# Kernel tuning notes

Hardware: AMD Instinct MI355X
Metric: run time of the kernel (lower is better)

Reference implementation:

```python
import jax, jax.numpy as jnp
import numpy as np

EPS = 1e-5
RADIUS = 1.0

def bn(x, gamma, beta, axis=1):
    # inference-mode BatchNorm1d: running_mean=0, running_var=1
    shape = [1] * x.ndim
    shape[axis] = -1
    return x * (gamma / jnp.sqrt(1.0 + EPS)).reshape(shape) + beta.reshape(shape)

def pconv(x, w):
    # pointwise Conv1d (kernel_size=1): x [B,Cin,N], w [Cout,Cin]
    return jnp.einsum('oi,bin->bon', w, x)

def sq_dist(a, b):
    # a [B,N,3], b [B,S,3] -> squared pairwise distances [B,N,S]
    return (jnp.sum(a * a, -1)[:, :, None] + jnp.sum(b * b, -1)[:, None, :]
            - 2.0 * jnp.einsum('bnc,bsc->bns', a, b))

def index_points(points, idx):
    # points [B,S,...], idx [B,...] -> gathered [B, idx.shape[1:], ...]
    return jax.vmap(lambda p, i: p[i])(points, idx)

def fps(xyz, npoint):
    # farthest point sampling (deterministic start at index 0)
    B, N, _ = xyz.shape
    binds = jnp.arange(B)
    def step(carry, _):
        dist, far = carry
        c = xyz[binds, far]                                    # [B,3]
        d = jnp.sum((xyz - c[:, None, :]) ** 2, -1)            # [B,N]
        dist = jnp.minimum(dist, d)
        nxt = jnp.argmax(dist, -1).astype(jnp.int32)
        return (dist, nxt), far
    init = (jnp.full((B, N), 1e10, xyz.dtype), jnp.zeros((B,), jnp.int32))
    _, idx = jax.lax.scan(step, init, None, length=npoint)
    return jnp.transpose(idx)                                   # [B,npoint]

def query_ball(radius, nsample, xyz, new_xyz):
    # indices of first nsample points within radius of each center
    B, N, _ = xyz.shape
    S = new_xyz.shape[1]
    d2 = sq_dist(new_xyz, xyz)                                  # [B,S,N]
    gidx = jnp.broadcast_to(jnp.arange(N, dtype=jnp.int32), (B, S, N))
    gidx = jnp.where(d2 > radius * radius, N, gidx)
    gidx = jnp.sort(gidx, axis=-1)[:, :, :nsample]
    first = gidx[:, :, :1]
    gidx = jnp.where(gidx == N, first, gidx)
    return jnp.clip(gidx, 0, N - 1)

def sample_and_group(npoint, nsample, radius, xyz, points):
    fps_idx = fps(xyz, npoint)
    new_xyz = index_points(xyz, fps_idx)                        # [B,S,3]
    new_pts = index_points(points, fps_idx)                     # [B,S,D]
    idx = query_ball(radius, nsample, xyz, new_xyz)             # [B,S,K]
    grouped = index_points(points, idx)                         # [B,S,K,D]
    centered = grouped - new_pts[:, :, None, :]
    rep = jnp.broadcast_to(new_pts[:, :, None, :], centered.shape)
    return new_xyz, jnp.concatenate([centered, rep], axis=-1)   # [B,S,K,2D]

def local_op(x, w1, g1, b1, w2, g2, b2):
    # x [B,n,K,d]; shared pointwise MLP over channels then max over K
    h = jnp.einsum('oi,bnki->bnok', w1, x)
    h = jax.nn.relu(bn(h, g1, b1, axis=2))
    h = jnp.einsum('oi,bnik->bnok', w2, h)
    h = jax.nn.relu(bn(h, g2, b2, axis=2))
    return jnp.transpose(jnp.max(h, -1), (0, 2, 1))             # [B,out,n]

def feature_prop(xyz1, xyz2, points1, points2, w1, g1, b1, w2, g2, b2):
    # 3-NN inverse-distance interpolation of points2 onto xyz1, concat points1
    p1 = jnp.transpose(xyz1, (0, 2, 1))                         # [B,N,3]
    p2 = jnp.transpose(xyz2, (0, 2, 1))                         # [B,S,3]
    f2 = jnp.transpose(points2, (0, 2, 1))                      # [B,S,D2]
    negd, idx = jax.lax.top_k(-sq_dist(p1, p2), 3)              # [B,N,3]
    recip = 1.0 / (-negd + 1e-8)
    w = recip / jnp.sum(recip, -1, keepdims=True)
    interp = jnp.sum(index_points(f2, idx) * w[..., None], 2)   # [B,N,D2]
    new = jnp.concatenate([points1, jnp.transpose(interp, (0, 2, 1))], axis=1)
    new = jax.nn.relu(bn(pconv(new, w1), g1, b1))
    new = jax.nn.relu(bn(pconv(new, w2), g2, b2))
    return new


def setup_inputs() -> dict:
    key = jax.random.key(0)
    ks = iter(jax.random.split(key, 80))
    def W(*s):  return jax.random.normal(next(ks), s, jnp.float32) * 0.05
    def G(n):   return 1.0 + 0.1 * jax.random.normal(next(ks), (n,), jnp.float32)
    def Bt(n):  return 0.1 * jax.random.normal(next(ks), (n,), jnp.float32)
    inp = {"x": jax.random.uniform(next(ks), (4, 8192, 3), jnp.float32)}
    inp.update(w_emb1=W(64, 3), g_emb1=G(64), be_emb1=Bt(64),
               w_emb2=W(64, 64), g_emb2=G(64), be_emb2=Bt(64),
               l0_w1=W(128, 128), l0_g1=G(128), l0_b1=Bt(128),
               l0_w2=W(128, 128), l0_g2=G(128), l0_b2=Bt(128),
               l1_w1=W(256, 256), l1_g1=G(256), l1_b1=Bt(256),
               l1_w2=W(256, 256), l1_g2=G(256), l1_b2=Bt(256),
               f0_w1=W(256, 384), f0_g1=G(256), f0_b1=Bt(256),
               f0_w2=W(512, 256), f0_g2=G(512), f0_b2=Bt(512),
               f1_w1=W(512, 576), f1_g1=G(512), f1_b1=Bt(512),
               f1_w2=W(1024, 512), f1_g2=G(1024), f1_b2=Bt(1024),
               c1_w=W(512, 1024), c1_bias=Bt(512), c1_g=G(512), c1_beta=Bt(512),
               c2_w=W(128, 512), c2_bias=Bt(128), c2_g=G(128), c2_beta=Bt(128),
               out_w=W(8, 128), out_bias=Bt(8))
    return inp


def reference(x, w_emb1, g_emb1, be_emb1, w_emb2, g_emb2, be_emb2,
              l0_w1, l0_g1, l0_b1, l0_w2, l0_g2, l0_b2,
              l1_w1, l1_g1, l1_b1, l1_w2, l1_g2, l1_b2,
              f0_w1, f0_g1, f0_b1, f0_w2, f0_g2, f0_b2,
              f1_w1, f1_g1, f1_b1, f1_w2, f1_g2, f1_b2,
              c1_w, c1_bias, c1_g, c1_beta, c2_w, c2_bias, c2_g, c2_beta,
              out_w, out_bias):
    xyz = x                                                     # [B,N,3]
    h = jnp.transpose(x, (0, 2, 1))                             # [B,3,N]
    h = jax.nn.relu(bn(pconv(h, w_emb1), g_emb1, be_emb1))
    h = jax.nn.relu(bn(pconv(h, w_emb2), g_emb2, be_emb2))
    feats0 = h                                                  # [B,64,N]
    xyz1, g1f = sample_and_group(2048, 32, RADIUS, xyz, jnp.transpose(h, (0, 2, 1)))
    feats1 = local_op(g1f, l0_w1, l0_g1, l0_b1, l0_w2, l0_g2, l0_b2)   # [B,128,2048]
    xyz2, g2f = sample_and_group(1024, 32, RADIUS, xyz1, jnp.transpose(feats1, (0, 2, 1)))
    feats2 = local_op(g2f, l1_w1, l1_g1, l1_b1, l1_w2, l1_g2, l1_b2)   # [B,256,1024]
    h = feature_prop(jnp.transpose(xyz1, (0, 2, 1)), jnp.transpose(xyz2, (0, 2, 1)),
                     feats1, feats2, f0_w1, f0_g1, f0_b1, f0_w2, f0_g2, f0_b2)   # [B,512,2048]
    h = feature_prop(jnp.transpose(xyz, (0, 2, 1)), jnp.transpose(xyz1, (0, 2, 1)),
                     feats0, h, f1_w1, f1_g1, f1_b1, f1_w2, f1_g2, f1_b2)        # [B,1024,N]
    h = jax.nn.relu(bn(pconv(h, c1_w) + c1_bias[None, :, None], c1_g, c1_beta))
    h = jax.nn.relu(bn(pconv(h, c2_w) + c2_bias[None, :, None], c2_g, c2_beta))
    logits = pconv(h, out_w) + out_bias[None, :, None]
    return jnp.transpose(logits, (0, 2, 1))                     # [B,N,labels]
```

## Files before the change

### kernel.cpp

```cpp
#include <hip/hip_runtime.h>
#include <math.h>


static constexpr size_t O_FEATS0 = 0;
static constexpr size_t O_FEATS1 = 8388608;
static constexpr size_t O_FEATS2 = 12582912;
static constexpr size_t O_FP0OUT = 16777216;
static constexpr size_t O_XYZ1   = 33554432;
static constexpr size_t O_XYZ2   = 33652736;
static constexpr size_t O_FPS1   = 33701888;
static constexpr size_t O_FPS2   = 33734656;
static constexpr size_t O_BALL1  = 33751040;
static constexpr size_t O_BALL2  = 34799616;
static constexpr size_t O_NN0I   = 35323904;
static constexpr size_t O_NN0W   = 35422208;
static constexpr size_t O_NN1I   = 35520512;
static constexpr size_t O_NN1W   = 35913728;
static constexpr size_t O_REG0   = 36306944;
static constexpr size_t O_REG1   = 103415808;
static constexpr size_t WS_NEED  = 170524672;

typedef float v2f __attribute__((ext_vector_type(2)));

__global__ __launch_bounds__(256) void emb_kernel(
    const float* __restrict__ xyz, const float* __restrict__ w1,
    const float* __restrict__ g1, const float* __restrict__ b1,
    const float* __restrict__ w2, const float* __restrict__ g2,
    const float* __restrict__ b2, float* __restrict__ out) {
  const int t = threadIdx.x;
  const int o = t & 63, pl = t >> 6;
  const int pt = blockIdx.x * 4 + pl;
  const float x0 = xyz[(size_t)pt * 3 + 0];
  const float x1 = xyz[(size_t)pt * 3 + 1];
  const float x2 = xyz[(size_t)pt * 3 + 2];
  const float SQ = sqrtf(1.0f + 1e-5f);
  float v = w1[o * 3 + 0] * x0 + w1[o * 3 + 1] * x1 + w1[o * 3 + 2] * x2;
  v = fmaxf(v * (g1[o] / SQ) + b1[o], 0.0f);
  __shared__ float h[4][64];
  h[pl][o] = v;
  __syncthreads();
  float acc = 0.0f;
  #pragma unroll 8
  for (int i = 0; i < 64; ++i) acc += w2[o * 64 + i] * h[pl][i];
  float y = fmaxf(acc * (g2[o] / SQ) + b2[o], 0.0f);
  out[(size_t)pt * 64 + o] = y;
}

__device__ __forceinline__ unsigned long long u64max(unsigned long long a,
                                                     unsigned long long b) {
  return a > b ? a : b;
}
template <int CTRL>
__device__ __forceinline__ unsigned long long dpp_step(unsigned long long k) {
  const int lo = (int)(unsigned)k;
  const int hi = (int)(unsigned)(k >> 32);
  const int nlo = __builtin_amdgcn_update_dpp(lo, lo, CTRL, 0xf, 0xf, false);
  const int nhi = __builtin_amdgcn_update_dpp(hi, hi, CTRL, 0xf, 0xf, false);
  return ((unsigned long long)(unsigned)nhi << 32) | (unsigned)nlo;
}

template <int N, int NP>
__global__ __launch_bounds__(256, 1) void fps_kernel(
    const float* __restrict__ xyz, int* __restrict__ out,
    float* __restrict__ oxyz) {
  #pragma clang fp contract(off)
  constexpr int PPT = N / 256;
  constexpr int PAIRS = PPT / 2;
  const int b = blockIdx.x, t = threadIdx.x;
  const float* xb = xyz + (size_t)b * N * 3;
  __shared__ float sx[N], sy[N], sz[N];
  __shared__ int sfar[NP];
  __shared__ unsigned long long skey[2][4];
  for (int i = t; i < N; i += 256) {
    sx[i] = xb[i * 3 + 0];
    sy[i] = xb[i * 3 + 1];
    sz[i] = xb[i * 3 + 2];
  }
  __syncthreads();
  v2f px[PAIRS], py[PAIRS], pz[PAIRS], ds[PAIRS];
  #pragma unroll
  for (int k = 0; k < PAIRS; ++k) {
    const int g = t * PPT + 2 * k;
    px[k].x = sx[g]; px[k].y = sx[g + 1];
    py[k].x = sy[g]; py[k].y = sy[g + 1];
    pz[k].x = sz[g]; pz[k].y = sz[g + 1];
    ds[k].x = 1e10f; ds[k].y = 1e10f;
  }
  const int wid = t >> 6, lane = t & 63;
  int far = 0;
  float ccx = sx[0], ccy = sy[0], ccz = sz[0];
  for (int it = 0; it < NP; ++it) {
    if (t == 0) sfar[it] = far;
    v2f cx2, cy2, cz2;
    cx2.x = ccx; cx2.y = ccx;
    cy2.x = ccy; cy2.y = ccy;
    cz2.x = ccz; cz2.y = ccz;
    #pragma unroll
    for (int k = 0; k < PAIRS; ++k) {
      const v2f dx = px[k] - cx2;
      const v2f dy = py[k] - cy2;
      const v2f dz = pz[k] - cz2;
      const v2f d = dx * dx + dy * dy + dz * dz;
      v2f nd;
      nd.x = fminf(ds[k].x, d.x);
      nd.y = fminf(ds[k].y, d.y);
      ds[k] = nd;
    }
    v2f tv[PAIRS / 2];
    #pragma unroll
    for (int k = 0; k < PAIRS / 2; ++k) {
      tv[k].x = fmaxf(ds[k].x, ds[k + PAIRS / 2].x);
      tv[k].y = fmaxf(ds[k].y, ds[k + PAIRS / 2].y);
    }
    #pragma unroll
    for (int w = PAIRS / 4; w >= 1; w >>= 1) {
      #pragma unroll
      for (int k = 0; k < w; ++k) {
        tv[k].x = fmaxf(tv[k].x, tv[k + w].x);
        tv[k].y = fmaxf(tv[k].y, tv[k + w].y);
      }
    }
    const float bv = fmaxf(tv[0].x, tv[0].y);
    unsigned mask = 0u;
    #pragma unroll
    for (int k = 0; k < PAIRS; ++k) {
      mask |= (ds[k].x == bv) ? (1u << (2 * k)) : 0u;
      mask |= (ds[k].y == bv) ? (1u << (2 * k + 1)) : 0u;
    }
    const int bjl = __builtin_ctz(mask);
    unsigned long long bk =
        ((unsigned long long)__float_as_uint(bv) << 32) |
        (unsigned long long)(unsigned)(~(unsigned)(t * PPT + bjl));
    bk = u64max(bk, dpp_step<0x111>(bk));
    bk = u64max(bk, dpp_step<0x112>(bk));
    bk = u64max(bk, dpp_step<0x114>(bk));
    bk = u64max(bk, dpp_step<0x118>(bk));
    bk = u64max(bk, dpp_step<0x142>(bk));
    bk = u64max(bk, dpp_step<0x143>(bk));
    const int p = it & 1;
    if (lane == 63) skey[p][wid] = bk;
    __syncthreads();
    unsigned long long wk = skey[p][0];
    #pragma unroll
    for (int q = 1; q < 4; ++q) {
      const unsigned long long k2 = skey[p][q];
      wk = (k2 > wk) ? k2 : wk;
    }
    far = (int)(~(unsigned)wk);
    ccx = sx[far]; ccy = sy[far]; ccz = sz[far];
  }
  __syncthreads();
  for (int i = t; i < NP; i += 256) {
    const int n = sfar[i];
    out[(size_t)b * NP + i] = n;
    oxyz[((size_t)b * NP + i) * 3 + 0] = sx[n];
    oxyz[((size_t)b * NP + i) * 3 + 1] = sy[n];
    oxyz[((size_t)b * NP + i) * 3 + 2] = sz[n];
  }
}

__global__ __launch_bounds__(256) void ball_kernel(
    const float* __restrict__ xyz, const float* __restrict__ ctr,
    int* __restrict__ out, int sbits, int N) {
  const int t = threadIdx.x;
  const int lane = t & 63, wid = t >> 6;
  const int wg = blockIdx.x * 4 + wid;
  const int b = wg >> sbits;
  __shared__ int lists[4][32];
  const float cx = ctr[(size_t)wg * 3 + 0];
  const float cy = ctr[(size_t)wg * 3 + 1];
  const float cz = ctr[(size_t)wg * 3 + 2];
  const float an = __fadd_rn(__fadd_rn(__fmul_rn(cx, cx), __fmul_rn(cy, cy)),
                             __fmul_rn(cz, cz));
  int fill = 0;
  for (int ch = 0; ch < (N >> 6) && fill < 32; ++ch) {
    const int n = ch * 64 + lane;
    const float bx = xyz[((size_t)b * N + n) * 3 + 0];
    const float by = xyz[((size_t)b * N + n) * 3 + 1];
    const float bz = xyz[((size_t)b * N + n) * 3 + 2];
    const float bb = __fadd_rn(__fadd_rn(__fmul_rn(bx, bx), __fmul_rn(by, by)),
                               __fmul_rn(bz, bz));
    const float dot = __fadd_rn(__fadd_rn(__fmul_rn(cx, bx), __fmul_rn(cy, by)),
                                __fmul_rn(cz, bz));
    const float d2 = __fsub_rn(__fadd_rn(an, bb), __fmul_rn(2.0f, dot));
    const bool q = (d2 <= 1.0f);
    const unsigned long long mask = __ballot(q);
    if (q) {
      const int pos = fill + __popcll(mask & ((1ull << lane) - 1ull));
      if (pos < 32) lists[wid][pos] = n;
    }
    fill += (int)__popcll(mask);
  }
  __syncthreads();
  if (lane < 32) {
    int v = lists[wid][0];
    if (lane < fill) v = lists[wid][lane];
    out[(size_t)wg * 32 + lane] = v;
  }
}

__global__ __launch_bounds__(256) void groupmat_kernel(
    float* __restrict__ Xo, const float* __restrict__ f,
    const int* __restrict__ ball, const int* __restrict__ fps, int g0, int Cf,
    int c4bits, int sbits, int Npts) {
  const int id = blockIdx.x * 256 + threadIdx.x;
  const int c4mask = (1 << c4bits) - 1;
  const int row = id >> c4bits;
  const int col = (id & c4mask) * 4;
  const int gl = g0 + (row >> 5);
  const int k = row & 31;
  const int b = gl >> sbits;
  const int src = ball[(size_t)gl * 32 + k];
  const int ctr = fps[gl];
  const int C = Cf * 2;
  const float* fb = f + (size_t)b * Npts * Cf;
  float4 v;
  if (col < Cf) {
    const float4 a = *(const float4*)(fb + (size_t)src * Cf + col);
    const float4 c = *(const float4*)(fb + (size_t)ctr * Cf + col);
    v = make_float4(a.x - c.x, a.y - c.y, a.z - c.z, a.w - c.w);
  } else {
    v = *(const float4*)(fb + (size_t)ctr * Cf + (col - Cf));
  }
  *(float4*)(Xo + (size_t)row * C + col) = v;
}

#define CMAP(c) ((((c) >> 3) * 12) + ((c) & 7))
__global__ __launch_bounds__(256) void conv_kernel(
    const float* __restrict__ X, const float* __restrict__ W,
    float* __restrict__ Y, int C, int O, const float* __restrict__ gamma,
    const float* __restrict__ beta, const float* __restrict__ bias, int relu) {
  __shared__ float Xs[16][188];
  __shared__ float Ws[16][188];
  const int t = threadIdx.x;
  const size_t m0 = (size_t)blockIdx.x * 128;
  const int o0 = blockIdx.y * 128;
  const int r0 = t >> 2;
  const int cq0 = (t & 3) * 4;
  const int mq = t & 15, nq = t >> 4;
  const int ca = CMAP(r0), cb = CMAP(r0 + 64);
  v2f acc[8][4];
  #pragma unroll
  for (int i = 0; i < 8; ++i)
    #pragma unroll
    for (int j = 0; j < 4; ++j) acc[i][j] = (v2f){0.0f, 0.0f};

  for (int kk = 0; kk < C; kk += 16) {
    const float4 xa = *(const float4*)(X + (m0 + r0) * C + kk + cq0);
    const float4 xb = *(const float4*)(X + (m0 + r0 + 64) * C + kk + cq0);
    const float4 wa = *(const float4*)(W + (size_t)(o0 + r0) * C + kk + cq0);
    const float4 wb = *(const float4*)(W + (size_t)(o0 + r0 + 64) * C + kk + cq0);
    __syncthreads();
    Xs[cq0 + 0][ca] = xa.x; Xs[cq0 + 1][ca] = xa.y;
    Xs[cq0 + 2][ca] = xa.z; Xs[cq0 + 3][ca] = xa.w;
    Xs[cq0 + 0][cb] = xb.x; Xs[cq0 + 1][cb] = xb.y;
    Xs[cq0 + 2][cb] = xb.z; Xs[cq0 + 3][cb] = xb.w;
    Ws[cq0 + 0][ca] = wa.x; Ws[cq0 + 1][ca] = wa.y;
    Ws[cq0 + 2][ca] = wa.z; Ws[cq0 + 3][ca] = wa.w;
    Ws[cq0 + 0][cb] = wb.x; Ws[cq0 + 1][cb] = wb.y;
    Ws[cq0 + 2][cb] = wb.z; Ws[cq0 + 3][cb] = wb.w;
    __syncthreads();
    #pragma unroll
    for (int k = 0; k < 16; ++k) {
      const float4 a0 = *(const float4*)&Xs[k][mq * 12];
      const float4 a1 = *(const float4*)&Xs[k][mq * 12 + 4];
      const float4 b0 = *(const float4*)&Ws[k][nq * 12];
      const float4 b1 = *(const float4*)&Ws[k][nq * 12 + 4];
      const float am[8] = {a0.x, a0.y, a0.z, a0.w, a1.x, a1.y, a1.z, a1.w};
      v2f bv[4];
      bv[0] = (v2f){b0.x, b0.y};
      bv[1] = (v2f){b0.z, b0.w};
      bv[2] = (v2f){b1.x, b1.y};
      bv[3] = (v2f){b1.z, b1.w};
      #pragma unroll
      for (int i = 0; i < 8; ++i) {
        const v2f as = (v2f){am[i], am[i]};
        #pragma unroll
        for (int j = 0; j < 4; ++j) acc[i][j] += as * bv[j];
      }
    }
  }

  const float SQ = sqrtf(1.0f + 1e-5f);
  float s[8], sh[8];
  #pragma unroll
  for (int j = 0; j < 8; ++j) {
    const int o = o0 + nq * 8 + j;
    const float sc = gamma ? (gamma[o] / SQ) : 1.0f;
    float bb = beta ? beta[o] : 0.0f;
    if (bias) bb = bb + bias[o] * sc;
    s[j] = sc; sh[j] = bb;
  }
  #pragma unroll
  for (int i = 0; i < 8; ++i) {
    float y[8];
    #pragma unroll
    for (int j = 0; j < 4; ++j) {
      float va = acc[i][j].x * s[2 * j] + sh[2 * j];
      float vb = acc[i][j].y * s[2 * j + 1] + sh[2 * j + 1];
      y[2 * j] = relu ? fmaxf(va, 0.0f) : va;
      y[2 * j + 1] = relu ? fmaxf(vb, 0.0f) : vb;
    }
    const size_t off = (m0 + mq * 8 + i) * O + o0 + nq * 8;
    *(float4*)(Y + off) = make_float4(y[0], y[1], y[2], y[3]);
    *(float4*)(Y + off + 4) = make_float4(y[4], y[5], y[6], y[7]);
  }
}

__global__ __launch_bounds__(256) void segmax_kernel(
    const float* __restrict__ Y, float* __restrict__ F, int O, int obits) {
  const int id = blockIdx.x * 256 + threadIdx.x;
  const int g = id >> obits;
  const int o = id & (O - 1);
  float m = -3.4e38f;
  #pragma unroll 8
  for (int k = 0; k < 32; ++k)
    m = fmaxf(m, Y[((size_t)g * 32 + k) * O + o]);
  F[(size_t)g * O + o] = m;
}

__global__ __launch_bounds__(256) void nn3_kernel(
    const float* __restrict__ txyz, const float* __restrict__ sxyz,
    int* __restrict__ oi, float* __restrict__ ow, int s1bits, int S2) {
  __shared__ float ss[6144];
  const int t = threadIdx.x;
  const int row = blockIdx.x * 256 + t;
  const int b = row >> s1bits;
  for (int i = t; i < S2 * 3; i += 256) ss[i] = sxyz[(size_t)b * S2 * 3 + i];
  __syncthreads();
  const float ax = txyz[(size_t)row * 3 + 0];
  const float ay = txyz[(size_t)row * 3 + 1];
  const float az = txyz[(size_t)row * 3 + 2];
  const float an = __fadd_rn(__fadd_rn(__fmul_rn(ax, ax), __fmul_rn(ay, ay)),
                             __fmul_rn(az, az));
  float d0 = 3.4e38f, d1 = 3.4e38f, d2v = 3.4e38f;
  int i0 = 0, i1 = 0, i2 = 0;
  for (int j = 0; j < S2; ++j) {
    const float bx = ss[j * 3 + 0], by = ss[j * 3 + 1], bz = ss[j * 3 + 2];
    const float bb = __fadd_rn(__fadd_rn(__fmul_rn(bx, bx), __fmul_rn(by, by)),
                               __fmul_rn(bz, bz));
    const float dot = __fadd_rn(__fadd_rn(__fmul_rn(ax, bx), __fmul_rn(ay, by)),
                                __fmul_rn(az, bz));
    const float dd = __fsub_rn(__fadd_rn(an, bb), __fmul_rn(2.0f, dot));
    if (dd < d0) {
      d2v = d1; i2 = i1; d1 = d0; i1 = i0; d0 = dd; i0 = j;
    } else if (dd < d1) {
      d2v = d1; i2 = i1; d1 = dd; i1 = j;
    } else if (dd < d2v) {
      d2v = dd; i2 = j;
    }
  }
  const float r0 = 1.0f / (d0 + 1e-8f);
  const float r1 = 1.0f / (d1 + 1e-8f);
  const float r2 = 1.0f / (d2v + 1e-8f);
  const float sum = __fadd_rn(__fadd_rn(r0, r1), r2);
  oi[(size_t)row * 3 + 0] = i0;
  oi[(size_t)row * 3 + 1] = i1;
  oi[(size_t)row * 3 + 2] = i2;
  ow[(size_t)row * 3 + 0] = r0 / sum;
  ow[(size_t)row * 3 + 1] = r1 / sum;
  ow[(size_t)row * 3 + 2] = r2 / sum;
}

__global__ __launch_bounds__(256) void interp_kernel(
    float* __restrict__ dst, int CT, int c0, const float* __restrict__ src,
    const int* __restrict__ idx, const float* __restrict__ w, int csbits,
    int s1bits, int S2) {
  const int id = blockIdx.x * 256 + threadIdx.x;
  const int row = id >> csbits;
  const int c4 = (id & ((1 << csbits) - 1)) * 4;
  const int Cs = 4 << csbits;
  const int b = row >> s1bits;
  const int j0 = idx[(size_t)row * 3 + 0];
  const int j1 = idx[(size_t)row * 3 + 1];
  const int j2 = idx[(size_t)row * 3 + 2];
  const float w0 = w[(size_t)row * 3 + 0];
  const float w1 = w[(size_t)row * 3 + 1];
  const float w2 = w[(size_t)row * 3 + 2];
  const float4 f0 = *(const float4*)(src + ((size_t)b * S2 + j0) * Cs + c4);
  const float4 f1 = *(const float4*)(src + ((size_t)b * S2 + j1) * Cs + c4);
  const float4 f2 = *(const float4*)(src + ((size_t)b * S2 + j2) * Cs + c4);
  float4 v;
  v.x = f0.x * w0 + f1.x * w1 + f2.x * w2;
  v.y = f0.y * w0 + f1.y * w1 + f2.y * w2;
  v.z = f0.z * w0 + f1.z * w1 + f2.z * w2;
  v.w = f0.w * w0 + f1.w * w1 + f2.w * w2;
  *(float4*)(dst + (size_t)row * CT + c0 + c4) = v;
}

__global__ __launch_bounds__(256) void copycols_kernel(
    float* __restrict__ dst, int CT, int c0, const float* __restrict__ src,
    int csbits) {
  const int id = blockIdx.x * 256 + threadIdx.x;
  const int row = id >> csbits;
  const int c4 = (id & ((1 << csbits) - 1)) * 4;
  const int Cs = 4 << csbits;
  const float4 v = *(const float4*)(src + (size_t)row * Cs + c4);
  *(float4*)(dst + (size_t)row * CT + c0 + c4) = v;
}

__global__ __launch_bounds__(256) void outfinal_kernel(
    const float* __restrict__ X, const float* __restrict__ Wt,
    const float* __restrict__ bias, float* __restrict__ out) {
  __shared__ float Xs[32][132];
  const int t = threadIdx.x;
  const int p0 = blockIdx.x * 32;
  #pragma unroll
  for (int q = 0; q < 4; ++q) {
    const int id = t + q * 256;
    const int r = id >> 5, c4 = (id & 31) * 4;
    const float4 v = *(const float4*)(X + (size_t)(p0 + r) * 128 + c4);
    Xs[r][c4 + 0] = v.x; Xs[r][c4 + 1] = v.y;
    Xs[r][c4 + 2] = v.z; Xs[r][c4 + 3] = v.w;
  }
  __syncthreads();
  const int p = t >> 3, o = t & 7;
  float acc = 0.0f;
  #pragma unroll 8
  for (int i = 0; i < 128; ++i) acc += Wt[o * 128 + i] * Xs[p][i];
  out[(size_t)(p0 + p) * 8 + o] = acc + bias[o];
}

extern "C" void kernel_launch(void* const* d_in, const int* in_sizes, int n_in,
                              void* d_out, int out_size, void* d_ws,
                              size_t ws_size, hipStream_t stream) {
  const float* x       = (const float*)d_in[0];
  const float* w_emb1  = (const float*)d_in[1];
  const float* g_emb1  = (const float*)d_in[2];
  const float* be_emb1 = (const float*)d_in[3];
  const float* w_emb2  = (const float*)d_in[4];
  const float* g_emb2  = (const float*)d_in[5];
  const float* be_emb2 = (const float*)d_in[6];
  const float* l0_w1 = (const float*)d_in[7];
  const float* l0_g1 = (const float*)d_in[8];
  const float* l0_b1 = (const float*)d_in[9];
  const float* l0_w2 = (const float*)d_in[10];
  const float* l0_g2 = (const float*)d_in[11];
  const float* l0_b2 = (const float*)d_in[12];
  const float* l1_w1 = (const float*)d_in[13];
  const float* l1_g1 = (const float*)d_in[14];
  const float* l1_b1 = (const float*)d_in[15];
  const float* l1_w2 = (const float*)d_in[16];
  const float* l1_g2 = (const float*)d_in[17];
  const float* l1_b2 = (const float*)d_in[18];
  const float* f0_w1 = (const float*)d_in[19];
  const float* f0_g1 = (const float*)d_in[20];
  const float* f0_b1 = (const float*)d_in[21];
  const float* f0_w2 = (const float*)d_in[22];
  const float* f0_g2 = (const float*)d_in[23];
  const float* f0_b2 = (const float*)d_in[24];
  const float* f1_w1 = (const float*)d_in[25];
  const float* f1_g1 = (const float*)d_in[26];
  const float* f1_b1 = (const float*)d_in[27];
  const float* f1_w2 = (const float*)d_in[28];
  const float* f1_g2 = (const float*)d_in[29];
  const float* f1_b2 = (const float*)d_in[30];
  const float* c1_w    = (const float*)d_in[31];
  const float* c1_bias = (const float*)d_in[32];
  const float* c1_g    = (const float*)d_in[33];
  const float* c1_beta = (const float*)d_in[34];
  const float* c2_w    = (const float*)d_in[35];
  const float* c2_bias = (const float*)d_in[36];
  const float* c2_g    = (const float*)d_in[37];
  const float* c2_beta = (const float*)d_in[38];
  const float* out_w    = (const float*)d_in[39];
  const float* out_bias = (const float*)d_in[40];

  if (ws_size < WS_NEED) return;

  char* ws = (char*)d_ws;
  float* feats0 = (float*)(ws + O_FEATS0);
  float* feats1 = (float*)(ws + O_FEATS1);
  float* feats2 = (float*)(ws + O_FEATS2);
  float* fp0out = (float*)(ws + O_FP0OUT);
  float* xyz1   = (float*)(ws + O_XYZ1);
  float* xyz2   = (float*)(ws + O_XYZ2);
  int*   fps1   = (int*)(ws + O_FPS1);
  int*   fps2   = (int*)(ws + O_FPS2);
  int*   ball1  = (int*)(ws + O_BALL1);
  int*   ball2  = (int*)(ws + O_BALL2);
  int*   nn0i   = (int*)(ws + O_NN0I);
  float* nn0w   = (float*)(ws + O_NN0W);
  int*   nn1i   = (int*)(ws + O_NN1I);
  float* nn1w   = (float*)(ws + O_NN1W);
  float* REG0   = (float*)(ws + O_REG0);
  float* REG1   = (float*)(ws + O_REG1);
  float* outp   = (float*)d_out;
  hipStream_t s = stream;

  emb_kernel<<<8192, 256, 0, s>>>(x, w_emb1, g_emb1, be_emb1, w_emb2, g_emb2,
                                  be_emb2, feats0);

  fps_kernel<8192, 2048><<<4, 256, 0, s>>>(x, fps1, xyz1);
  ball_kernel<<<2048, 256, 0, s>>>(x, xyz1, ball1, 11, 8192);
  for (int c = 0; c < 2; ++c) {
    groupmat_kernel<<<16384, 256, 0, s>>>(REG0, feats0, ball1, fps1, c * 4096,
                                          64, 5, 11, 8192);
    conv_kernel<<<dim3(1024, 1), 256, 0, s>>>(REG0, l0_w1, REG1, 128, 128,
                                              l0_g1, l0_b1, nullptr, 1);
    conv_kernel<<<dim3(1024, 1), 256, 0, s>>>(REG1, l0_w2, REG0, 128, 128,
                                              l0_g2, l0_b2, nullptr, 1);
    segmax_kernel<<<2048, 256, 0, s>>>(REG0, feats1 + (size_t)c * 4096 * 128,
                                       128, 7);
  }

  fps_kernel<2048, 1024><<<4, 256, 0, s>>>(xyz1, fps2, xyz2);
  ball_kernel<<<1024, 256, 0, s>>>(xyz1, xyz2, ball2, 10, 2048);
  for (int c = 0; c < 2; ++c) {
    groupmat_kernel<<<16384, 256, 0, s>>>(REG0, feats1, ball2, fps2, c * 2048,
                                          128, 6, 10, 2048);
    conv_kernel<<<dim3(512, 2), 256, 0, s>>>(REG0, l1_w1, REG1, 256, 256,
                                             l1_g1, l1_b1, nullptr, 1);
    conv_kernel<<<dim3(512, 2), 256, 0, s>>>(REG1, l1_w2, REG0, 256, 256,
                                             l1_g2, l1_b2, nullptr, 1);
    segmax_kernel<<<2048, 256, 0, s>>>(REG0, feats2 + (size_t)c * 2048 * 256,
                                       256, 8);
  }

  nn3_kernel<<<32, 256, 0, s>>>(xyz1, xyz2, nn0i, nn0w, 11, 1024);
  copycols_kernel<<<1024, 256, 0, s>>>(REG0, 384, 0, feats1, 5);
  interp_kernel<<<2048, 256, 0, s>>>(REG0, 384, 128, feats2, nn0i, nn0w, 6, 11,
                                     1024);
  conv_kernel<<<dim3(64, 2), 256, 0, s>>>(REG0, f0_w1, REG1, 384, 256, f0_g1,
                                          f0_b1, nullptr, 1);
  conv_kernel<<<dim3(64, 4), 256, 0, s>>>(REG1, f0_w2, fp0out, 256, 512, f0_g2,
                                          f0_b2, nullptr, 1);

  nn3_kernel<<<128, 256, 0, s>>>(x, xyz1, nn1i, nn1w, 13, 2048);
  for (int b = 0; b < 4; b += 2) {
    copycols_kernel<<<1024, 256, 0, s>>>(REG0, 576, 0,
                                         feats0 + (size_t)b * 8192 * 64, 4);
    interp_kernel<<<8192, 256, 0, s>>>(REG0, 576, 64,
                                       fp0out + (size_t)b * 2048 * 512,
                                       nn1i + (size_t)b * 8192 * 3,
                                       nn1w + (size_t)b * 8192 * 3, 7, 13,
                                       2048);
    conv_kernel<<<dim3(128, 4), 256, 0, s>>>(REG0, f1_w1, REG1, 576, 512,
                                             f1_g1, f1_b1, nullptr, 1);
    conv_kernel<<<dim3(128, 8), 256, 0, s>>>(REG1, f1_w2, REG0, 512, 1024,
                                             f1_g2, f1_b2, nullptr, 1);
    conv_kernel<<<dim3(128, 4), 256, 0, s>>>(REG0, c1_w, REG1, 1024, 512,
                                             c1_g, c1_beta, c1_bias, 1);
    conv_kernel<<<dim3(128, 1), 256, 0, s>>>(REG1, c2_w, REG0, 512, 128,
                                             c2_g, c2_beta, c2_bias, 1);
    outfinal_kernel<<<512, 256, 0, s>>>(REG0, out_w, out_bias,
                                        outp + (size_t)b * 8192 * 8);
  }
}
```

Baseline: 4.995 ms.

## Fuse group gather into conv, segmax into second conv, co-launch emb/fps and ball/nn

Folds the grouping gather into the first local conv so the grouped matrix is never written to global memory. Folds the segment max into the epilogue of the second conv so the full per-neighbour output is never written. Runs the embedding MLP as extra blocks of the FPS launch so it fills the idle CUs while four FPS blocks run serially. Ball query and 3-NN are merged into one launch in the same way. This removes several large global round trips and launches, but the conv tile's X load now becomes an indirect gather, and FPS shares a launch with many short blocks.

```diff
diff --git a/kernel.cpp b/kernel.cpp
--- a/kernel.cpp
+++ b/kernel.cpp
@@ -22,30 +22,6 @@
 
 typedef float v2f __attribute__((ext_vector_type(2)));
 
-__global__ __launch_bounds__(256) void emb_kernel(
-    const float* __restrict__ xyz, const float* __restrict__ w1,
-    const float* __restrict__ g1, const float* __restrict__ b1,
-    const float* __restrict__ w2, const float* __restrict__ g2,
-    const float* __restrict__ b2, float* __restrict__ out) {
-  const int t = threadIdx.x;
-  const int o = t & 63, pl = t >> 6;
-  const int pt = blockIdx.x * 4 + pl;
-  const float x0 = xyz[(size_t)pt * 3 + 0];
-  const float x1 = xyz[(size_t)pt * 3 + 1];
-  const float x2 = xyz[(size_t)pt * 3 + 2];
-  const float SQ = sqrtf(1.0f + 1e-5f);
-  float v = w1[o * 3 + 0] * x0 + w1[o * 3 + 1] * x1 + w1[o * 3 + 2] * x2;
-  v = fmaxf(v * (g1[o] / SQ) + b1[o], 0.0f);
-  __shared__ float h[4][64];
-  h[pl][o] = v;
-  __syncthreads();
-  float acc = 0.0f;
-  #pragma unroll 8
-  for (int i = 0; i < 64; ++i) acc += w2[o * 64 + i] * h[pl][i];
-  float y = fmaxf(acc * (g2[o] / SQ) + b2[o], 0.0f);
-  out[(size_t)pt * 64 + o] = y;
-}
-
 __device__ __forceinline__ unsigned long long u64max(unsigned long long a,
                                                      unsigned long long b) {
   return a > b ? a : b;
@@ -59,18 +35,47 @@
   return ((unsigned long long)(unsigned)nhi << 32) | (unsigned)nlo;
 }
 
-template <int N, int NP>
+template <int N, int NP, bool EMB>
 __global__ __launch_bounds__(256, 1) void fps_kernel(
     const float* __restrict__ xyz, int* __restrict__ out,
-    float* __restrict__ oxyz) {
+    float* __restrict__ oxyz, const float* __restrict__ w1,
+    const float* __restrict__ g1, const float* __restrict__ b1,
+    const float* __restrict__ w2, const float* __restrict__ g2,
+    const float* __restrict__ b2, float* __restrict__ femb) {
   #pragma clang fp contract(off)
   constexpr int PPT = N / 256;
   constexpr int PAIRS = PPT / 2;
-  const int b = blockIdx.x, t = threadIdx.x;
-  const float* xb = xyz + (size_t)b * N * 3;
   __shared__ float sx[N], sy[N], sz[N];
   __shared__ int sfar[NP];
   __shared__ unsigned long long skey[2][4];
+
+  if constexpr (EMB) {
+    if (blockIdx.x >= 4) {
+      #pragma clang fp contract(fast)
+      const int bid = blockIdx.x - 4;
+      const int t = threadIdx.x;
+      const int o = t & 63, pl = t >> 6;
+      const int pt = bid * 4 + pl;
+      const float x0 = xyz[(size_t)pt * 3 + 0];
+      const float x1 = xyz[(size_t)pt * 3 + 1];
+      const float x2 = xyz[(size_t)pt * 3 + 2];
+      const float SQ = sqrtf(1.0f + 1e-5f);
+      float v = w1[o * 3 + 0] * x0 + w1[o * 3 + 1] * x1 + w1[o * 3 + 2] * x2;
+      v = fmaxf(v * (g1[o] / SQ) + b1[o], 0.0f);
+      float* h = sx;
+      h[pl * 64 + o] = v;
+      __syncthreads();
+      float acc = 0.0f;
+      #pragma unroll 8
+      for (int i = 0; i < 64; ++i) acc += w2[o * 64 + i] * h[pl * 64 + i];
+      float y = fmaxf(acc * (g2[o] / SQ) + b2[o], 0.0f);
+      femb[(size_t)pt * 64 + o] = y;
+      return;
+    }
+  }
+
+  const int b = blockIdx.x, t = threadIdx.x;
+  const float* xb = xyz + (size_t)b * N * 3;
   for (int i = t; i < N; i += 256) {
     sx[i] = xb[i * 3 + 0];
     sy[i] = xb[i * 3 + 1];
@@ -159,172 +164,51 @@
   }
 }
 
-__global__ __launch_bounds__(256) void ball_kernel(
-    const float* __restrict__ xyz, const float* __restrict__ ctr,
-    int* __restrict__ out, int sbits, int N) {
-  const int t = threadIdx.x;
-  const int lane = t & 63, wid = t >> 6;
-  const int wg = blockIdx.x * 4 + wid;
-  const int b = wg >> sbits;
-  __shared__ int lists[4][32];
-  const float cx = ctr[(size_t)wg * 3 + 0];
-  const float cy = ctr[(size_t)wg * 3 + 1];
-  const float cz = ctr[(size_t)wg * 3 + 2];
-  const float an = __fadd_rn(__fadd_rn(__fmul_rn(cx, cx), __fmul_rn(cy, cy)),
-                             __fmul_rn(cz, cz));
-  int fill = 0;
-  for (int ch = 0; ch < (N >> 6) && fill < 32; ++ch) {
-    const int n = ch * 64 + lane;
-    const float bx = xyz[((size_t)b * N + n) * 3 + 0];
-    const float by = xyz[((size_t)b * N + n) * 3 + 1];
-    const float bz = xyz[((size_t)b * N + n) * 3 + 2];
-    const float bb = __fadd_rn(__fadd_rn(__fmul_rn(bx, bx), __fmul_rn(by, by)),
-                               __fmul_rn(bz, bz));
-    const float dot = __fadd_rn(__fadd_rn(__fmul_rn(cx, bx), __fmul_rn(cy, by)),
-                                __fmul_rn(cz, bz));
-    const float d2 = __fsub_rn(__fadd_rn(an, bb), __fmul_rn(2.0f, dot));
-    const bool q = (d2 <= 1.0f);
-    const unsigned long long mask = __ballot(q);
-    if (q) {
-      const int pos = fill + __popcll(mask & ((1ull << lane) - 1ull));
-      if (pos < 32) lists[wid][pos] = n;
-    }
-    fill += (int)__popcll(mask);
-  }
-  __syncthreads();
-  if (lane < 32) {
-    int v = lists[wid][0];
-    if (lane < fill) v = lists[wid][lane];
-    out[(size_t)wg * 32 + lane] = v;
-  }
-}
-
-__global__ __launch_bounds__(256) void groupmat_kernel(
-    float* __restrict__ Xo, const float* __restrict__ f,
-    const int* __restrict__ ball, const int* __restrict__ fps, int g0, int Cf,
-    int c4bits, int sbits, int Npts) {
-  const int id = blockIdx.x * 256 + threadIdx.x;
-  const int c4mask = (1 << c4bits) - 1;
-  const int row = id >> c4bits;
-  const int col = (id & c4mask) * 4;
-  const int gl = g0 + (row >> 5);
-  const int k = row & 31;
-  const int b = gl >> sbits;
-  const int src = ball[(size_t)gl * 32 + k];
-  const int ctr = fps[gl];
-  const int C = Cf * 2;
-  const float* fb = f + (size_t)b * Npts * Cf;
-  float4 v;
-  if (col < Cf) {
-    const float4 a = *(const float4*)(fb + (size_t)src * Cf + col);
-    const float4 c = *(const float4*)(fb + (size_t)ctr * Cf + col);
-    v = make_float4(a.x - c.x, a.y - c.y, a.z - c.z, a.w - c.w);
-  } else {
-    v = *(const float4*)(fb + (size_t)ctr * Cf + (col - Cf));
-  }
-  *(float4*)(Xo + (size_t)row * C + col) = v;
-}
-
-#define CMAP(c) ((((c) >> 3) * 12) + ((c) & 7))
-__global__ __launch_bounds__(256) void conv_kernel(
-    const float* __restrict__ X, const float* __restrict__ W,
-    float* __restrict__ Y, int C, int O, const float* __restrict__ gamma,
-    const float* __restrict__ beta, const float* __restrict__ bias, int relu) {
-  __shared__ float Xs[16][188];
-  __shared__ float Ws[16][188];
-  const int t = threadIdx.x;
-  const size_t m0 = (size_t)blockIdx.x * 128;
-  const int o0 = blockIdx.y * 128;
-  const int r0 = t >> 2;
-  const int cq0 = (t & 3) * 4;
-  const int mq = t & 15, nq = t >> 4;
-  const int ca = CMAP(r0), cb = CMAP(r0 + 64);
-  v2f acc[8][4];
-  #pragma unroll
-  for (int i = 0; i < 8; ++i)
-    #pragma unroll
-    for (int j = 0; j < 4; ++j) acc[i][j] = (v2f){0.0f, 0.0f};
-
-  for (int kk = 0; kk < C; kk += 16) {
-    const float4 xa = *(const float4*)(X + (m0 + r0) * C + kk + cq0);
-    const float4 xb = *(const float4*)(X + (m0 + r0 + 64) * C + kk + cq0);
-    const float4 wa = *(const float4*)(W + (size_t)(o0 + r0) * C + kk + cq0);
-    const float4 wb = *(const float4*)(W + (size_t)(o0 + r0 + 64) * C + kk + cq0);
-    __syncthreads();
-    Xs[cq0 + 0][ca] = xa.x; Xs[cq0 + 1][ca] = xa.y;
-    Xs[cq0 + 2][ca] = xa.z; Xs[cq0 + 3][ca] = xa.w;
-    Xs[cq0 + 0][cb] = xb.x; Xs[cq0 + 1][cb] = xb.y;
-    Xs[cq0 + 2][cb] = xb.z; Xs[cq0 + 3][cb] = xb.w;
-    Ws[cq0 + 0][ca] = wa.x; Ws[cq0 + 1][ca] = wa.y;
-    Ws[cq0 + 2][ca] = wa.z; Ws[cq0 + 3][ca] = wa.w;
-    Ws[cq0 + 0][cb] = wb.x; Ws[cq0 + 1][cb] = wb.y;
-    Ws[cq0 + 2][cb] = wb.z; Ws[cq0 + 3][cb] = wb.w;
-    __syncthreads();
-    #pragma unroll
-    for (int k = 0; k < 16; ++k) {
-      const float4 a0 = *(const float4*)&Xs[k][mq * 12];
-      const float4 a1 = *(const float4*)&Xs[k][mq * 12 + 4];
-      const float4 b0 = *(const float4*)&Ws[k][nq * 12];
-      const float4 b1 = *(const float4*)&Ws[k][nq * 12 + 4];
-      const float am[8] = {a0.x, a0.y, a0.z, a0.w, a1.x, a1.y, a1.z, a1.w};
-      v2f bv[4];
-      bv[0] = (v2f){b0.x, b0.y};
-      bv[1] = (v2f){b0.z, b0.w};
-      bv[2] = (v2f){b1.x, b1.y};
-      bv[3] = (v2f){b1.z, b1.w};
-      #pragma unroll
-      for (int i = 0; i < 8; ++i) {
-        const v2f as = (v2f){am[i], am[i]};
-        #pragma unroll
-        for (int j = 0; j < 4; ++j) acc[i][j] += as * bv[j];
-      }
-    }
-  }
-
-  const float SQ = sqrtf(1.0f + 1e-5f);
-  float s[8], sh[8];
-  #pragma unroll
-  for (int j = 0; j < 8; ++j) {
-    const int o = o0 + nq * 8 + j;
-    const float sc = gamma ? (gamma[o] / SQ) : 1.0f;
-    float bb = beta ? beta[o] : 0.0f;
-    if (bias) bb = bb + bias[o] * sc;
-    s[j] = sc; sh[j] = bb;
-  }
-  #pragma unroll
-  for (int i = 0; i < 8; ++i) {
-    float y[8];
-    #pragma unroll
-    for (int j = 0; j < 4; ++j) {
-      float va = acc[i][j].x * s[2 * j] + sh[2 * j];
-      float vb = acc[i][j].y * s[2 * j + 1] + sh[2 * j + 1];
-      y[2 * j] = relu ? fmaxf(va, 0.0f) : va;
-      y[2 * j + 1] = relu ? fmaxf(vb, 0.0f) : vb;
-    }
-    const size_t off = (m0 + mq * 8 + i) * O + o0 + nq * 8;
-    *(float4*)(Y + off) = make_float4(y[0], y[1], y[2], y[3]);
-    *(float4*)(Y + off + 4) = make_float4(y[4], y[5], y[6], y[7]);
-  }
-}
-
-__global__ __launch_bounds__(256) void segmax_kernel(
-    const float* __restrict__ Y, float* __restrict__ F, int O, int obits) {
-  const int id = blockIdx.x * 256 + threadIdx.x;
-  const int g = id >> obits;
-  const int o = id & (O - 1);
-  float m = -3.4e38f;
-  #pragma unroll 8
-  for (int k = 0; k < 32; ++k)
-    m = fmaxf(m, Y[((size_t)g * 32 + k) * O + o]);
-  F[(size_t)g * O + o] = m;
-}
-
-__global__ __launch_bounds__(256) void nn3_kernel(
+__global__ __launch_bounds__(256) void ballnn_kernel(
+    const float* __restrict__ cloud, const float* __restrict__ ctr,
+    int* __restrict__ ballOut, int sbits, int N, int nBallBlk,
     const float* __restrict__ txyz, const float* __restrict__ sxyz,
     int* __restrict__ oi, float* __restrict__ ow, int s1bits, int S2) {
+  __shared__ int lists[4][32];
   __shared__ float ss[6144];
   const int t = threadIdx.x;
-  const int row = blockIdx.x * 256 + t;
+  if ((int)blockIdx.x < nBallBlk) {
+    const int lane = t & 63, wid = t >> 6;
+    const int wg = blockIdx.x * 4 + wid;
+    const int b = wg >> sbits;
+    const float cx = ctr[(size_t)wg * 3 + 0];
+    const float cy = ctr[(size_t)wg * 3 + 1];
+    const float cz = ctr[(size_t)wg * 3 + 2];
+    const float an = __fadd_rn(__fadd_rn(__fmul_rn(cx, cx), __fmul_rn(cy, cy)),
+                               __fmul_rn(cz, cz));
+    int fill = 0;
+    for (int ch = 0; ch < (N >> 6) && fill < 32; ++ch) {
+      const int n = ch * 64 + lane;
+      const float bx = cloud[((size_t)b * N + n) * 3 + 0];
+      const float by = cloud[((size_t)b * N + n) * 3 + 1];
+      const float bz = cloud[((size_t)b * N + n) * 3 + 2];
+      const float bb = __fadd_rn(
+          __fadd_rn(__fmul_rn(bx, bx), __fmul_rn(by, by)), __fmul_rn(bz, bz));
+      const float dot = __fadd_rn(
+          __fadd_rn(__fmul_rn(cx, bx), __fmul_rn(cy, by)), __fmul_rn(cz, bz));
+      const float d2 = __fsub_rn(__fadd_rn(an, bb), __fmul_rn(2.0f, dot));
+      const bool q = (d2 <= 1.0f);
+      const unsigned long long mask = __ballot(q);
+      if (q) {
+        const int pos = fill + __popcll(mask & ((1ull << lane) - 1ull));
+        if (pos < 32) lists[wid][pos] = n;
+      }
+      fill += (int)__popcll(mask);
+    }
+    __syncthreads();
+    if (lane < 32) {
+      int v = lists[wid][0];
+      if (lane < fill) v = lists[wid][lane];
+      ballOut[(size_t)wg * 32 + lane] = v;
+    }
+    return;
+  }
+  const int row = (blockIdx.x - nBallBlk) * 256 + t;
   const int b = row >> s1bits;
   for (int i = t; i < S2 * 3; i += 256) ss[i] = sxyz[(size_t)b * S2 * 3 + i];
   __syncthreads();
@@ -360,6 +244,291 @@
   ow[(size_t)row * 3 + 0] = r0 / sum;
   ow[(size_t)row * 3 + 1] = r1 / sum;
   ow[(size_t)row * 3 + 2] = r2 / sum;
+}
+
+#define CMAP(c) ((((c) >> 3) * 12) + ((c) & 7))
+
+__global__ __launch_bounds__(256) void conv_gather_kernel(
+    const float* __restrict__ f, const int* __restrict__ ball,
+    const int* __restrict__ fps, int g0, int Cf, int sbits, int Npts,
+    const float* __restrict__ W, float* __restrict__ Y, int O,
+    const float* __restrict__ gamma, const float* __restrict__ beta) {
+  const int C = Cf * 2;
+  __shared__ float Xs[16][188];
+  __shared__ float Ws[16][188];
+  const int t = threadIdx.x;
+  const size_t m0 = (size_t)blockIdx.x * 128;
+  const int o0 = blockIdx.y * 128;
+  const int r0 = t >> 2;
+  const int cq0 = (t & 3) * 4;
+  const int mq = t & 15, nq = t >> 4;
+  const int ca = CMAP(r0), cb = CMAP(r0 + 64);
+  const int mA = (int)m0 + r0, mB = (int)m0 + r0 + 64;
+  const int glA = g0 + (mA >> 5), glB = g0 + (mB >> 5);
+  const int srcA = ball[(size_t)glA * 32 + (mA & 31)];
+  const int srcB = ball[(size_t)glB * 32 + (mB & 31)];
+  const int ctrA = fps[glA], ctrB = fps[glB];
+  const float* fbA = f + (size_t)(glA >> sbits) * Npts * Cf;
+  const float* fbB = f + (size_t)(glB >> sbits) * Npts * Cf;
+  v2f acc[8][4];
+  #pragma unroll
+  for (int i = 0; i < 8; ++i)
+    #pragma unroll
+    for (int j = 0; j < 4; ++j) acc[i][j] = (v2f){0.0f, 0.0f};
+
+  for (int kk = 0; kk < C; kk += 16) {
+    const int col = kk + cq0;
+    const bool lo = col < Cf;
+    const int col2 = lo ? col : col - Cf;
+    float4 xa, xb;
+    {
+      const float4 c4 = *(const float4*)(fbA + (size_t)ctrA * Cf + col2);
+      if (lo) {
+        const float4 s4 = *(const float4*)(fbA + (size_t)srcA * Cf + col);
+        xa = make_float4(s4.x - c4.x, s4.y - c4.y, s4.z - c4.z, s4.w - c4.w);
+      } else {
+        xa = c4;
+      }
+    }
+    {
+      const float4 c4 = *(const float4*)(fbB + (size_t)ctrB * Cf + col2);
+      if (lo) {
+        const float4 s4 = *(const float4*)(fbB + (size_t)srcB * Cf + col);
+        xb = make_float4(s4.x - c4.x, s4.y - c4.y, s4.z - c4.z, s4.w - c4.w);
+      } else {
+        xb = c4;
+      }
+    }
+    const float4 wa = *(const float4*)(W + (size_t)(o0 + r0) * C + kk + cq0);
+    const float4 wb =
+        *(const float4*)(W + (size_t)(o0 + r0 + 64) * C + kk + cq0);
+    __syncthreads();
+    Xs[cq0 + 0][ca] = xa.x; Xs[cq0 + 1][ca] = xa.y;
+    Xs[cq0 + 2][ca] = xa.z; Xs[cq0 + 3][ca] = xa.w;
+    Xs[cq0 + 0][cb] = xb.x; Xs[cq0 + 1][cb] = xb.y;
+    Xs[cq0 + 2][cb] = xb.z; Xs[cq0 + 3][cb] = xb.w;
+    Ws[cq0 + 0][ca] = wa.x; Ws[cq0 + 1][ca] = wa.y;
+    Ws[cq0 + 2][ca] = wa.z; Ws[cq0 + 3][ca] = wa.w;
+    Ws[cq0 + 0][cb] = wb.x; Ws[cq0 + 1][cb] = wb.y;
+    Ws[cq0 + 2][cb] = wb.z; Ws[cq0 + 3][cb] = wb.w;
+    __syncthreads();
+    #pragma unroll
+    for (int k = 0; k < 16; ++k) {
+      const float4 a0 = *(const float4*)&Xs[k][mq * 12];
+      const float4 a1 = *(const float4*)&Xs[k][mq * 12 + 4];
+      const float4 b0 = *(const float4*)&Ws[k][nq * 12];
+      const float4 b1 = *(const float4*)&Ws[k][nq * 12 + 4];
+      const float am[8] = {a0.x, a0.y, a0.z, a0.w, a1.x, a1.y, a1.z, a1.w};
+      v2f bv[4];
+      bv[0] = (v2f){b0.x, b0.y};
+      bv[1] = (v2f){b0.z, b0.w};
+      bv[2] = (v2f){b1.x, b1.y};
+      bv[3] = (v2f){b1.z, b1.w};
+      #pragma unroll
+      for (int i = 0; i < 8; ++i) {
+        const v2f as = (v2f){am[i], am[i]};
+        #pragma unroll
+        for (int j = 0; j < 4; ++j) acc[i][j] += as * bv[j];
+      }
+    }
+  }
+
+  const float SQ = sqrtf(1.0f + 1e-5f);
+  float s[8], sh[8];
+  #pragma unroll
+  for (int j = 0; j < 8; ++j) {
+    const int o = o0 + nq * 8 + j;
+    s[j] = gamma[o] / SQ;
+    sh[j] = beta[o];
+  }
+  #pragma unroll
+  for (int i = 0; i < 8; ++i) {
+    float y[8];
+    #pragma unroll
+    for (int j = 0; j < 4; ++j) {
+      y[2 * j] = fmaxf(acc[i][j].x * s[2 * j] + sh[2 * j], 0.0f);
+      y[2 * j + 1] = fmaxf(acc[i][j].y * s[2 * j + 1] + sh[2 * j + 1], 0.0f);
+    }
+    const size_t off = (m0 + mq * 8 + i) * O + o0 + nq * 8;
+    *(float4*)(Y + off) = make_float4(y[0], y[1], y[2], y[3]);
+    *(float4*)(Y + off + 4) = make_float4(y[4], y[5], y[6], y[7]);
+  }
+}
+
+__global__ __launch_bounds__(256) void conv2sm_kernel(
+    const float* __restrict__ X, const float* __restrict__ W,
+    float* __restrict__ F, int C, int O, const float* __restrict__ gamma,
+    const float* __restrict__ beta) {
+  __shared__ float Xs[16][188];
+  __shared__ float Ws[16][188];
+  const int t = threadIdx.x;
+  const size_t m0 = (size_t)blockIdx.x * 128;
+  const int o0 = blockIdx.y * 128;
+  const int r0 = t >> 2;
+  const int cq0 = (t & 3) * 4;
+  const int mq = t & 15, nq = t >> 4;
+  const int ca = CMAP(r0), cb = CMAP(r0 + 64);
+  v2f acc[8][4];
+  #pragma unroll
+  for (int i = 0; i < 8; ++i)
+    #pragma unroll
+    for (int j = 0; j < 4; ++j) acc[i][j] = (v2f){0.0f, 0.0f};
+
+  for (int kk = 0; kk < C; kk += 16) {
+    const float4 xa = *(const float4*)(X + (m0 + r0) * C + kk + cq0);
+    const float4 xb = *(const float4*)(X + (m0 + r0 + 64) * C + kk + cq0);
+    const float4 wa = *(const float4*)(W + (size_t)(o0 + r0) * C + kk + cq0);
+    const float4 wb =
+        *(const float4*)(W + (size_t)(o0 + r0 + 64) * C + kk + cq0);
+    __syncthreads();
+    Xs[cq0 + 0][ca] = xa.x; Xs[cq0 + 1][ca] = xa.y;
+    Xs[cq0 + 2][ca] = xa.z; Xs[cq0 + 3][ca] = xa.w;
+    Xs[cq0 + 0][cb] = xb.x; Xs[cq0 + 1][cb] = xb.y;
+    Xs[cq0 + 2][cb] = xb.z; Xs[cq0 + 3][cb] = xb.w;
+    Ws[cq0 + 0][ca] = wa.x; Ws[cq0 + 1][ca] = wa.y;
+    Ws[cq0 + 2][ca] = wa.z; Ws[cq0 + 3][ca] = wa.w;
+    Ws[cq0 + 0][cb] = wb.x; Ws[cq0 + 1][cb] = wb.y;
+    Ws[cq0 + 2][cb] = wb.z; Ws[cq0 + 3][cb] = wb.w;
+    __syncthreads();
+    #pragma unroll
+    for (int k = 0; k < 16; ++k) {
+      const float4 a0 = *(const float4*)&Xs[k][mq * 12];
+      const float4 a1 = *(const float4*)&Xs[k][mq * 12 + 4];
+      const float4 b0 = *(const float4*)&Ws[k][nq * 12];
+      const float4 b1 = *(const float4*)&Ws[k][nq * 12 + 4];
+      const float am[8] = {a0.x, a0.y, a0.z, a0.w, a1.x, a1.y, a1.z, a1.w};
+      v2f bv[4];
+      bv[0] = (v2f){b0.x, b0.y};
+      bv[1] = (v2f){b0.z, b0.w};
+      bv[2] = (v2f){b1.x, b1.y};
+      bv[3] = (v2f){b1.z, b1.w};
+      #pragma unroll
+      for (int i = 0; i < 8; ++i) {
+        const v2f as = (v2f){am[i], am[i]};
+        #pragma unroll
+        for (int j = 0; j < 4; ++j) acc[i][j] += as * bv[j];
+      }
+    }
+  }
+
+  const float SQ = sqrtf(1.0f + 1e-5f);
+  float s[8], sh[8];
+  #pragma unroll
+  for (int j = 0; j < 8; ++j) {
+    const int o = o0 + nq * 8 + j;
+    s[j] = gamma[o] / SQ;
+    sh[j] = beta[o];
+  }
+  float colmax[8];
+  #pragma unroll
+  for (int j = 0; j < 8; ++j) colmax[j] = -3.4e38f;
+  #pragma unroll
+  for (int i = 0; i < 8; ++i) {
+    #pragma unroll
+    for (int j = 0; j < 4; ++j) {
+      const float va = fmaxf(acc[i][j].x * s[2 * j] + sh[2 * j], 0.0f);
+      const float vb = fmaxf(acc[i][j].y * s[2 * j + 1] + sh[2 * j + 1], 0.0f);
+      colmax[2 * j] = fmaxf(colmax[2 * j], va);
+      colmax[2 * j + 1] = fmaxf(colmax[2 * j + 1], vb);
+    }
+  }
+  __syncthreads();
+  float* smax = &Xs[0][0];
+  #pragma unroll
+  for (int j = 0; j < 8; ++j) smax[mq * 132 + nq * 8 + j] = colmax[j];
+  __syncthreads();
+  #pragma unroll
+  for (int q = 0; q < 2; ++q) {
+    const int idx = t + q * 256;
+    const int g = idx >> 7;
+    const int col = idx & 127;
+    const float m =
+        fmaxf(fmaxf(smax[(4 * g + 0) * 132 + col], smax[(4 * g + 1) * 132 + col]),
+              fmaxf(smax[(4 * g + 2) * 132 + col], smax[(4 * g + 3) * 132 + col]));
+    F[(size_t)(blockIdx.x * 4 + g) * O + o0 + col] = m;
+  }
+}
+
+__global__ __launch_bounds__(256) void conv_kernel(
+    const float* __restrict__ X, const float* __restrict__ W,
+    float* __restrict__ Y, int C, int O, const float* __restrict__ gamma,
+    const float* __restrict__ beta, const float* __restrict__ bias, int relu) {
+  __shared__ float Xs[16][188];
+  __shared__ float Ws[16][188];
+  const int t = threadIdx.x;
+  const size_t m0 = (size_t)blockIdx.x * 128;
+  const int o0 = blockIdx.y * 128;
+  const int r0 = t >> 2;
+  const int cq0 = (t & 3) * 4;
+  const int mq = t & 15, nq = t >> 4;
+  const int ca = CMAP(r0), cb = CMAP(r0 + 64);
+  v2f acc[8][4];
+  #pragma unroll
+  for (int i = 0; i < 8; ++i)
+    #pragma unroll
+    for (int j = 0; j < 4; ++j) acc[i][j] = (v2f){0.0f, 0.0f};
+
+  for (int kk = 0; kk < C; kk += 16) {
+    const float4 xa = *(const float4*)(X + (m0 + r0) * C + kk + cq0);
+    const float4 xb = *(const float4*)(X + (m0 + r0 + 64) * C + kk + cq0);
+    const float4 wa = *(const float4*)(W + (size_t)(o0 + r0) * C + kk + cq0);
+    const float4 wb =
+        *(const float4*)(W + (size_t)(o0 + r0 + 64) * C + kk + cq0);
+    __syncthreads();
+    Xs[cq0 + 0][ca] = xa.x; Xs[cq0 + 1][ca] = xa.y;
+    Xs[cq0 + 2][ca] = xa.z; Xs[cq0 + 3][ca] = xa.w;
+    Xs[cq0 + 0][cb] = xb.x; Xs[cq0 + 1][cb] = xb.y;
+    Xs[cq0 + 2][cb] = xb.z; Xs[cq0 + 3][cb] = xb.w;
+    Ws[cq0 + 0][ca] = wa.x; Ws[cq0 + 1][ca] = wa.y;
+    Ws[cq0 + 2][ca] = wa.z; Ws[cq0 + 3][ca] = wa.w;
+    Ws[cq0 + 0][cb] = wb.x; Ws[cq0 + 1][cb] = wb.y;
+    Ws[cq0 + 2][cb] = wb.z; Ws[cq0 + 3][cb] = wb.w;
+    __syncthreads();
+    #pragma unroll
+    for (int k = 0; k < 16; ++k) {
+      const float4 a0 = *(const float4*)&Xs[k][mq * 12];
+      const float4 a1 = *(const float4*)&Xs[k][mq * 12 + 4];
+      const float4 b0 = *(const float4*)&Ws[k][nq * 12];
+      const float4 b1 = *(const float4*)&Ws[k][nq * 12 + 4];
+      const float am[8] = {a0.x, a0.y, a0.z, a0.w, a1.x, a1.y, a1.z, a1.w};
+      v2f bv[4];
+      bv[0] = (v2f){b0.x, b0.y};
+      bv[1] = (v2f){b0.z, b0.w};
+      bv[2] = (v2f){b1.x, b1.y};
+      bv[3] = (v2f){b1.z, b1.w};
+      #pragma unroll
+      for (int i = 0; i < 8; ++i) {
+        const v2f as = (v2f){am[i], am[i]};
+        #pragma unroll
+        for (int j = 0; j < 4; ++j) acc[i][j] += as * bv[j];
+      }
+    }
+  }
+
+  const float SQ = sqrtf(1.0f + 1e-5f);
+  float s[8], sh[8];
+  #pragma unroll
+  for (int j = 0; j < 8; ++j) {
+    const int o = o0 + nq * 8 + j;
+    const float sc = gamma ? (gamma[o] / SQ) : 1.0f;
+    float bb = beta ? beta[o] : 0.0f;
+    if (bias) bb = bb + bias[o] * sc;
+    s[j] = sc; sh[j] = bb;
+  }
+  #pragma unroll
+  for (int i = 0; i < 8; ++i) {
+    float y[8];
+    #pragma unroll
+    for (int j = 0; j < 4; ++j) {
+      float va = acc[i][j].x * s[2 * j] + sh[2 * j];
+      float vb = acc[i][j].y * s[2 * j + 1] + sh[2 * j + 1];
+      y[2 * j] = relu ? fmaxf(va, 0.0f) : va;
+      y[2 * j + 1] = relu ? fmaxf(vb, 0.0f) : vb;
+    }
+    const size_t off = (m0 + mq * 8 + i) * O + o0 + nq * 8;
+    *(float4*)(Y + off) = make_float4(y[0], y[1], y[2], y[3]);
+    *(float4*)(Y + off + 4) = make_float4(y[4], y[5], y[6], y[7]);
+  }
 }
 
 __global__ __launch_bounds__(256) void interp_kernel(
@@ -488,36 +657,35 @@
   float* outp   = (float*)d_out;
   hipStream_t s = stream;
 
-  emb_kernel<<<8192, 256, 0, s>>>(x, w_emb1, g_emb1, be_emb1, w_emb2, g_emb2,
-                                  be_emb2, feats0);
-
-  fps_kernel<8192, 2048><<<4, 256, 0, s>>>(x, fps1, xyz1);
-  ball_kernel<<<2048, 256, 0, s>>>(x, xyz1, ball1, 11, 8192);
+  fps_kernel<8192, 2048, true><<<4 + 8192, 256, 0, s>>>(
+      x, fps1, xyz1, w_emb1, g_emb1, be_emb1, w_emb2, g_emb2, be_emb2, feats0);
+
+  ballnn_kernel<<<2048 + 128, 256, 0, s>>>(x, xyz1, ball1, 11, 8192, 2048,
+                                           x, xyz1, nn1i, nn1w, 13, 2048);
+
   for (int c = 0; c < 2; ++c) {
-    groupmat_kernel<<<16384, 256, 0, s>>>(REG0, feats0, ball1, fps1, c * 4096,
-                                          64, 5, 11, 8192);
-    conv_kernel<<<dim3(1024, 1), 256, 0, s>>>(REG0, l0_w1, REG1, 128, 128,
-                                              l0_g1, l0_b1, nullptr, 1);
-    conv_kernel<<<dim3(1024, 1), 256, 0, s>>>(REG1, l0_w2, REG0, 128, 128,
-                                              l0_g2, l0_b2, nullptr, 1);
-    segmax_kernel<<<2048, 256, 0, s>>>(REG0, feats1 + (size_t)c * 4096 * 128,
-                                       128, 7);
-  }
-
-  fps_kernel<2048, 1024><<<4, 256, 0, s>>>(xyz1, fps2, xyz2);
-  ball_kernel<<<1024, 256, 0, s>>>(xyz1, xyz2, ball2, 10, 2048);
+    conv_gather_kernel<<<dim3(1024, 1), 256, 0, s>>>(
+        feats0, ball1, fps1, c * 4096, 64, 11, 8192, l0_w1, REG1, 128, l0_g1,
+        l0_b1);
+    conv2sm_kernel<<<dim3(1024, 1), 256, 0, s>>>(
+        REG1, l0_w2, feats1 + (size_t)c * 4096 * 128, 128, 128, l0_g2, l0_b2);
+  }
+
+  fps_kernel<2048, 1024, false><<<4, 256, 0, s>>>(
+      xyz1, fps2, xyz2, nullptr, nullptr, nullptr, nullptr, nullptr, nullptr,
+      nullptr);
+
+  ballnn_kernel<<<1024 + 32, 256, 0, s>>>(xyz1, xyz2, ball2, 10, 2048, 1024,
+                                          xyz1, xyz2, nn0i, nn0w, 11, 1024);
+
   for (int c = 0; c < 2; ++c) {
-    groupmat_kernel<<<16384, 256, 0, s>>>(REG0, feats1, ball2, fps2, c * 2048,
-                                          128, 6, 10, 2048);
-    conv_kernel<<<dim3(512, 2), 256, 0, s>>>(REG0, l1_w1, REG1, 256, 256,
-                                             l1_g1, l1_b1, nullptr, 1);
-    conv_kernel<<<dim3(512, 2), 256, 0, s>>>(REG1, l1_w2, REG0, 256, 256,
-                                             l1_g2, l1_b2, nullptr, 1);
-    segmax_kernel<<<2048, 256, 0, s>>>(REG0, feats2 + (size_t)c * 2048 * 256,
-                                       256, 8);
-  }
-
-  nn3_kernel<<<32, 256, 0, s>>>(xyz1, xyz2, nn0i, nn0w, 11, 1024);
+    conv_gather_kernel<<<dim3(512, 2), 256, 0, s>>>(
+        feats1, ball2, fps2, c * 2048, 128, 10, 2048, l1_w1, REG1, 256, l1_g1,
+        l1_b1);
+    conv2sm_kernel<<<dim3(512, 2), 256, 0, s>>>(
+        REG1, l1_w2, feats2 + (size_t)c * 2048 * 256, 256, 256, l1_g2, l1_b2);
+  }
+
   copycols_kernel<<<1024, 256, 0, s>>>(REG0, 384, 0, feats1, 5);
   interp_kernel<<<2048, 256, 0, s>>>(REG0, 384, 128, feats2, nn0i, nn0w, 6, 11,
                                      1024);
@@ -526,7 +694,6 @@
   conv_kernel<<<dim3(64, 4), 256, 0, s>>>(REG1, f0_w2, fp0out, 256, 512, f0_g2,
                                           f0_b2, nullptr, 1);
 
-  nn3_kernel<<<128, 256, 0, s>>>(x, xyz1, nn1i, nn1w, 13, 2048);
   for (int b = 0; b < 4; b += 2) {
     copycols_kernel<<<1024, 256, 0, s>>>(REG0, 576, 0,
                                          feats0 + (size_t)b * 8192 * 64, 4);
```

After: 4.907 ms. No clear change (-1.8%).
